# Performance work log

Hardware: AMD Instinct MI355X
Metric: run time of the kernel (lower is better)

## Reference

```python
import jax, jax.numpy as jnp
import numpy as np

NEG = -1000000000.0


def setup_inputs() -> dict:
    key = jax.random.key(0)
    k1, k2, k3, k4, k5 = jax.random.split(key, 5)
    B, T, D, Q = 8, 2048, 1024, 128
    x = jax.random.normal(k1, (B, T, D), dtype=jnp.float32)
    attn_mask = jax.random.randint(k2, (B, T), 0, 2).astype(jnp.bool_)
    s = 1.0 / np.sqrt(D)
    Wq = jax.random.normal(k3, (Q, D), dtype=jnp.float32) * s
    Wk = jax.random.normal(k4, (Q, D), dtype=jnp.float32) * s
    Wv = jax.random.normal(k5, (Q, D), dtype=jnp.float32) * s
    return {"x": x, "attn_mask": attn_mask, "Wq": Wq, "Wk": Wk, "Wv": Wv}


def reference(x, attn_mask, Wq, Wk, Wv):
    # x: (B,T,D); W*: (Q,D) torch Linear weights (y = x @ W.T)
    q = jnp.einsum('btd,qd->btq', x, Wq)
    k = jnp.einsum('btd,qd->btq', x, Wk)
    v = jnp.einsum('btd,qd->btq', x, Wv)
    logits = jnp.einsum('btq,bsq->bts', q, k)  # (B,T,T), no 1/sqrt(d) scaling (matches source)
    m = attn_mask[:, None, :]  # (B,1,T) broadcasts over query dim, == repeat(1,T,1)
    logits = jnp.where(m, logits, NEG)
    A = jax.nn.softmax(logits, axis=-1)
    A = jnp.where(m, A, 0.0)
    return jnp.einsum('bts,bsq->btq', A, v)
```

## Files before the change

### kernel.cpp

```cpp
#include <hip/hip_runtime.h>
#include <hip/hip_bf16.h>
#include <hip/hip_fp16.h>

typedef _Float16 half8 __attribute__((ext_vector_type(8)));
typedef _Float16 half4v __attribute__((ext_vector_type(4)));
typedef float float4v __attribute__((ext_vector_type(4)));

#define MFMA_F16(a, b, c) __builtin_amdgcn_mfma_f32_16x16x32_f16((a), (b), (c), 0, 0, 0)

#define GLDS16(gp, lp) \
    __builtin_amdgcn_global_load_lds((const __attribute__((address_space(1))) unsigned int*)(gp), \
                                     (__attribute__((address_space(3))) unsigned int*)(lp), 16, 0, 0)

#define BATCH 8
#define SEQ   2048
#define DIM   1024
#define QD    128
#define BT    (BATCH * SEQ)
#define NSPLIT 4
#define KSPAN (SEQ / NSPLIT)

__device__ __forceinline__ float dpp_max16(float x) {
    int v;
    v = __builtin_amdgcn_update_dpp(0, __float_as_int(x), 0xB1, 0xF, 0xF, false);
    x = fmaxf(x, __int_as_float(v));
    v = __builtin_amdgcn_update_dpp(0, __float_as_int(x), 0x4E, 0xF, 0xF, false);
    x = fmaxf(x, __int_as_float(v));
    v = __builtin_amdgcn_update_dpp(0, __float_as_int(x), 0x141, 0xF, 0xF, false);
    x = fmaxf(x, __int_as_float(v));
    v = __builtin_amdgcn_update_dpp(0, __float_as_int(x), 0x140, 0xF, 0xF, false);
    x = fmaxf(x, __int_as_float(v));
    return x;
}

__global__ __launch_bounds__(256) void cvt_w_kernel(const float* __restrict__ Wq,
                                                    const float* __restrict__ Wk,
                                                    const float* __restrict__ Wv,
                                                    _Float16* __restrict__ Wh) {
    const float* src = (blockIdx.y == 0) ? Wq : ((blockIdx.y == 1) ? Wk : Wv);
    int i = blockIdx.x * 256 + threadIdx.x;
    float4 f = ((const float4*)src)[i];
    half4v h = {(_Float16)f.x, (_Float16)f.y, (_Float16)f.z, (_Float16)f.w};
    ((half4v*)(Wh + (size_t)blockIdx.y * QD * DIM))[i] = h;
}

__global__ __launch_bounds__(512, 1) void proj_kernel(
    const float* __restrict__ x,
    const _Float16* __restrict__ Wh,
    _Float16* __restrict__ q_out,
    _Float16* __restrict__ k_out,
    _Float16* __restrict__ vt_out)
{
    __shared__ _Float16 As[2][64 * 64];
    __shared__ _Float16 Bs[2][3 * 128 * 64];

    const int tid  = threadIdx.x;
    const int lane = tid & 63;
    const int wave = tid >> 6;
    const int quad = lane >> 4;
    const int l15  = lane & 15;
    const int wr   = wave >> 2;
    const int wcg  = wave & 3;

    const int row0 = blockIdx.x * 64;

    const int ar  = tid >> 3;
    const int ac8 = tid & 7;
    const float* xp = x + (size_t)(row0 + ar) * DIM + ac8 * 8;
    const int aslot = ar * 64 + ((ac8 ^ (ar & 7)) * 8);

    float4v acc[3][2][2];
#pragma unroll
    for (int m = 0; m < 3; m++)
#pragma unroll
        for (int rf = 0; rf < 2; rf++)
#pragma unroll
            for (int nf = 0; nf < 2; nf++)
                acc[m][rf][nf] = (float4v){0.f, 0.f, 0.f, 0.f};

    {
        float4 a0 = *(const float4*)(xp + 0);
        float4 a1 = *(const float4*)(xp + 4);
#pragma unroll
        for (int c = 0; c < 6; c++) {
            int ci = c * 512 + tid;
            int m  = ci >> 10;
            int ri = (ci >> 3) & 127;
            int gs = ci & 7;
            int g  = gs ^ (ri & 7);
            GLDS16(Wh + (size_t)m * QD * DIM + (size_t)ri * DIM + g * 8, &Bs[0][ci * 8]);
        }
        half8 h;
        h[0] = (_Float16)a0.x; h[1] = (_Float16)a0.y; h[2] = (_Float16)a0.z; h[3] = (_Float16)a0.w;
        h[4] = (_Float16)a1.x; h[5] = (_Float16)a1.y; h[6] = (_Float16)a1.z; h[7] = (_Float16)a1.w;
        *(half8*)&As[0][aslot] = h;
    }
    __syncthreads();

    for (int t = 0; t < 16; t++) {
        const int cur = t & 1;
        const int nxt = cur ^ 1;

        float4 b0, b1;
        if (t < 15) {
            const float* xq = xp + (t + 1) * 64;
            b0 = *(const float4*)(xq + 0);
            b1 = *(const float4*)(xq + 4);
            const int kkn = (t + 1) * 64;
#pragma unroll
            for (int c = 0; c < 6; c++) {
                int ci = c * 512 + tid;
                int m  = ci >> 10;
                int ri = (ci >> 3) & 127;
                int gs = ci & 7;
                int g  = gs ^ (ri & 7);
                GLDS16(Wh + (size_t)m * QD * DIM + (size_t)ri * DIM + kkn + g * 8,
                       &Bs[nxt][ci * 8]);
            }
        }

        half8 af[2][2];
#pragma unroll
        for (int rf = 0; rf < 2; rf++)
#pragma unroll
            for (int kc = 0; kc < 2; kc++) {
                int r = wr * 32 + rf * 16 + l15;
                int g = (kc * 4 + quad) ^ (r & 7);
                af[rf][kc] = *(const half8*)&As[cur][r * 64 + g * 8];
            }
#pragma unroll
        for (int m = 0; m < 3; m++) {
            half8 bf[2][2];
#pragma unroll
            for (int nf = 0; nf < 2; nf++)
#pragma unroll
                for (int kc = 0; kc < 2; kc++) {
                    int r = wcg * 32 + nf * 16 + l15;
                    int g = (kc * 4 + quad) ^ (r & 7);
                    bf[nf][kc] = *(const half8*)&Bs[cur][m * 8192 + r * 64 + g * 8];
                }
#pragma unroll
            for (int kc = 0; kc < 2; kc++)
#pragma unroll
                for (int rf = 0; rf < 2; rf++)
#pragma unroll
                    for (int nf = 0; nf < 2; nf++)
                        acc[m][rf][nf] = MFMA_F16(af[rf][kc], bf[nf][kc], acc[m][rf][nf]);
        }

        if (t < 15) {
            half8 h;
            h[0] = (_Float16)b0.x; h[1] = (_Float16)b0.y; h[2] = (_Float16)b0.z; h[3] = (_Float16)b0.w;
            h[4] = (_Float16)b1.x; h[5] = (_Float16)b1.y; h[6] = (_Float16)b1.z; h[7] = (_Float16)b1.w;
            *(half8*)&As[nxt][aslot] = h;
        }
        __syncthreads();
    }

#pragma unroll
    for (int m = 0; m < 3; m++) {
        if (m == 2) {
#pragma unroll
            for (int rf = 0; rf < 2; rf++) {
                int grow0 = row0 + wr * 32 + rf * 16 + quad * 4;
                int b  = grow0 >> 11;
                int t0 = grow0 & 2047;
#pragma unroll
                for (int nf = 0; nf < 2; nf++) {
                    int col = wcg * 32 + nf * 16 + l15;
                    half4v h;
#pragma unroll
                    for (int r = 0; r < 4; r++) h[r] = (_Float16)acc[m][rf][nf][r];
                    *(half4v*)&vt_out[((size_t)(b * QD + col)) * SEQ + t0] = h;
                }
            }
        } else {
            _Float16* out = (m == 0) ? q_out : k_out;
#pragma unroll
            for (int rf = 0; rf < 2; rf++) {
                int grow0 = row0 + wr * 32 + rf * 16 + quad * 4;
#pragma unroll
                for (int nf = 0; nf < 2; nf++) {
                    int col = wcg * 32 + nf * 16 + l15;
#pragma unroll
                    for (int r = 0; r < 4; r++)
                        out[(size_t)(grow0 + r) * QD + col] = (_Float16)acc[m][rf][nf][r];
                }
            }
        }
    }
}

__global__ __launch_bounds__(256, 2) void attn_kernel(
    const _Float16* __restrict__ q,
    const _Float16* __restrict__ k,
    const _Float16* __restrict__ vt,
    const int* __restrict__ mask,
    _Float16* __restrict__ Op,
    float2* __restrict__ ml)
{
    __shared__ _Float16 Ks[64 * 128];
    __shared__ _Float16 Vs[128 * 64];
    __shared__ _Float16 Ps[4 * 32 * 64];
    __shared__ float Msf[64];

    const int tid  = threadIdx.x;
    const int lane = tid & 63;
    const int wave = tid >> 6;
    const int quad = lane >> 4;
    const int l15  = lane & 15;

    const int b  = blockIdx.y;
    const int z  = blockIdx.z;
    const int rowbase = blockIdx.x * 128 + wave * 32;

    half8 qf[2][4];
#pragma unroll
    for (int rf = 0; rf < 2; rf++) {
        const _Float16* qrow = q + ((size_t)(b * SEQ + rowbase + rf * 16 + l15)) * QD + quad * 8;
#pragma unroll
        for (int kc = 0; kc < 4; kc++)
            qf[rf][kc] = *(const half8*)(qrow + kc * 32);
    }

    const half8 onesv = {(_Float16)1, (_Float16)1, (_Float16)1, (_Float16)1,
                         (_Float16)1, (_Float16)1, (_Float16)1, (_Float16)1};

    float4v oacc[2][8];
#pragma unroll
    for (int rf = 0; rf < 2; rf++)
#pragma unroll
        for (int n = 0; n < 8; n++)
            oacc[rf][n] = (float4v){0.f, 0.f, 0.f, 0.f};
    float4v lacc[2] = {(float4v){0.f, 0.f, 0.f, 0.f}, (float4v){0.f, 0.f, 0.f, 0.f}};
    float mrow[2][4];
#pragma unroll
    for (int rf = 0; rf < 2; rf++)
#pragma unroll
        for (int r = 0; r < 4; r++) mrow[rf][r] = -1e30f;

    _Float16* Pw = &Ps[wave * 32 * 64];

    for (int sb = z * KSPAN; sb < z * KSPAN + KSPAN; sb += 64) {
        __syncthreads();
#pragma unroll
        for (int c = 0; c < 4; c++) {
            int ci = wave * 256 + c * 64 + lane;
            int r  = ci >> 4;
            int gs = ci & 15;
            int g  = (gs & 8) | ((gs ^ r) & 7);
            GLDS16(k + ((size_t)(b * SEQ + sb + r)) * QD + g * 8, &Ks[(wave * 256 + c * 64) * 8]);
        }
#pragma unroll
        for (int c = 0; c < 4; c++) {
            int ci = wave * 256 + c * 64 + lane;
            int r  = ci >> 3;
            int g  = ((ci & 7) ^ r) & 7;
            GLDS16(vt + ((size_t)(b * QD + r)) * SEQ + sb + g * 8, &Vs[(wave * 256 + c * 64) * 8]);
        }
        if (tid < 64) Msf[tid] = mask[b * SEQ + sb + tid] ? 0.f : -1e30f;
        __syncthreads();

        float4v sacc[2][4];
#pragma unroll
        for (int rf = 0; rf < 2; rf++)
#pragma unroll
            for (int j = 0; j < 4; j++)
                sacc[rf][j] = (float4v){0.f, 0.f, 0.f, 0.f};
#pragma unroll
        for (int kc = 0; kc < 4; kc++) {
            half8 kf[4];
#pragma unroll
            for (int j = 0; j < 4; j++) {
                int r  = j * 16 + l15;
                int g  = kc * 4 + quad;
                int gs = (g & 8) | ((g ^ r) & 7);
                kf[j] = *(const half8*)&Ks[r * 128 + gs * 8];
            }
#pragma unroll
            for (int rf = 0; rf < 2; rf++)
#pragma unroll
                for (int j = 0; j < 4; j++)
                    sacc[rf][j] = MFMA_F16(qf[rf][kc], kf[j], sacc[rf][j]);
        }

        float alpha[2][4];
#pragma unroll
        for (int rf = 0; rf < 2; rf++) {
            float rmax[4] = {-1e30f, -1e30f, -1e30f, -1e30f};
#pragma unroll
            for (int j = 0; j < 4; j++) {
                float bias = Msf[j * 16 + l15];
#pragma unroll
                for (int r = 0; r < 4; r++) {
                    float s = sacc[rf][j][r] + bias;
                    sacc[rf][j][r] = s;
                    rmax[r] = fmaxf(rmax[r], s);
                }
            }
#pragma unroll
            for (int r = 0; r < 4; r++) {
                float rm = dpp_max16(rmax[r]);
                float mnew = fmaxf(mrow[rf][r], rm);
                alpha[rf][r] = __expf(mrow[rf][r] - mnew);
                mrow[rf][r] = mnew;
            }
        }

#pragma unroll
        for (int rf = 0; rf < 2; rf++)
#pragma unroll
            for (int j = 0; j < 4; j++) {
                int col = j * 16 + l15;
                int gc  = col >> 3;
#pragma unroll
                for (int r = 0; r < 4; r++) {
                    int m  = rf * 16 + quad * 4 + r;
                    int gs = (gc ^ m) & 7;
                    float p = __expf(sacc[rf][j][r] - mrow[rf][r]);
                    Pw[m * 64 + gs * 8 + (col & 7)] = (_Float16)p;
                }
            }

#pragma unroll
        for (int rf = 0; rf < 2; rf++) {
#pragma unroll
            for (int n = 0; n < 8; n++)
#pragma unroll
                for (int r = 0; r < 4; r++)
                    oacc[rf][n][r] *= alpha[rf][r];
#pragma unroll
            for (int r = 0; r < 4; r++) lacc[rf][r] *= alpha[rf][r];
        }

#pragma unroll
        for (int kc = 0; kc < 2; kc++) {
            half8 pf[2];
#pragma unroll
            for (int rf = 0; rf < 2; rf++) {
                int m  = rf * 16 + l15;
                int gs = ((kc * 4 + quad) ^ m) & 7;
                pf[rf] = *(const half8*)&Pw[m * 64 + gs * 8];
            }
#pragma unroll
            for (int n = 0; n < 8; n++) {
                int r  = n * 16 + l15;
                int gs = ((kc * 4 + quad) ^ r) & 7;
                half8 vf = *(const half8*)&Vs[r * 64 + gs * 8];
#pragma unroll
                for (int rf = 0; rf < 2; rf++)
                    oacc[rf][n] = MFMA_F16(pf[rf], vf, oacc[rf][n]);
            }
#pragma unroll
            for (int rf = 0; rf < 2; rf++)
                lacc[rf] = MFMA_F16(pf[rf], onesv, lacc[rf]);
        }
    }

    _Float16* Oz = Op + (size_t)z * BT * QD;
#pragma unroll
    for (int rf = 0; rf < 2; rf++) {
#pragma unroll
        for (int n = 0; n < 8; n++) {
            int col = n * 16 + l15;
#pragma unroll
            for (int r = 0; r < 4; r++) {
                int row = rowbase + rf * 16 + quad * 4 + r;
                Oz[((size_t)(b * SEQ + row)) * QD + col] = (_Float16)oacc[rf][n][r];
            }
        }
        if (l15 == 0) {
#pragma unroll
            for (int r = 0; r < 4; r++) {
                int row = rowbase + rf * 16 + quad * 4 + r;
                ml[(size_t)z * BT + b * SEQ + row] = make_float2(mrow[rf][r], lacc[rf][r]);
            }
        }
    }
}

__global__ __launch_bounds__(256) void merge_kernel(
    const _Float16* __restrict__ Op,
    const float2* __restrict__ ml,
    float* __restrict__ out)
{
    int gid = blockIdx.x * 256 + threadIdx.x;
    int row = gid >> 4;
    int c8  = (gid & 15) * 8;

    float2 a[NSPLIT];
    float m = -3.0e38f;
#pragma unroll
    for (int s = 0; s < NSPLIT; s++) { a[s] = ml[(size_t)s * BT + row]; m = fmaxf(m, a[s].x); }
    float sc[NSPLIT];
    float denom = 0.f;
#pragma unroll
    for (int s = 0; s < NSPLIT; s++) { sc[s] = __expf(a[s].x - m); denom += sc[s] * a[s].y; }
    float inv = (denom > 0.f) ? (1.0f / denom) : 0.f;

    float acc[8] = {0, 0, 0, 0, 0, 0, 0, 0};
#pragma unroll
    for (int s = 0; s < NSPLIT; s++) {
        half8 o = *(const half8*)&Op[(size_t)s * BT * QD + (size_t)row * QD + c8];
#pragma unroll
        for (int e = 0; e < 8; e++) acc[e] += (float)o[e] * sc[s];
    }
    float4 lo = make_float4(acc[0] * inv, acc[1] * inv, acc[2] * inv, acc[3] * inv);
    float4 hi = make_float4(acc[4] * inv, acc[5] * inv, acc[6] * inv, acc[7] * inv);
    *(float4*)&out[(size_t)row * QD + c8] = lo;
    *(float4*)&out[(size_t)row * QD + c8 + 4] = hi;
}

extern "C" void kernel_launch(void* const* d_in, const int* in_sizes, int n_in,
                              void* d_out, int out_size, void* d_ws, size_t ws_size,
                              hipStream_t stream) {
    const float* x    = (const float*)d_in[0];
    const int*   mask = (const int*)d_in[1];
    const float* Wq   = (const float*)d_in[2];
    const float* Wk   = (const float*)d_in[3];
    const float* Wv   = (const float*)d_in[4];
    float* out = (float*)d_out;

    char* p = (char*)d_ws;
    _Float16* Wh  = (_Float16*)p; p += (size_t)3 * QD * DIM * 2;
    _Float16* qb  = (_Float16*)p; p += (size_t)BT * QD * 2;
    _Float16* kb  = (_Float16*)p; p += (size_t)BT * QD * 2;
    _Float16* vtb = (_Float16*)p; p += (size_t)BT * QD * 2;
    _Float16* Op  = (_Float16*)p; p += (size_t)NSPLIT * BT * QD * 2;
    float2*   ml  = (float2*)p;

    cvt_w_kernel<<<dim3(QD * DIM / 4 / 256, 3), 256, 0, stream>>>(Wq, Wk, Wv, Wh);
    proj_kernel<<<dim3(BT / 64), 512, 0, stream>>>(x, Wh, qb, kb, vtb);
    attn_kernel<<<dim3(SEQ / 128, BATCH, NSPLIT), 256, 0, stream>>>(qb, kb, vtb, mask, Op, ml);
    merge_kernel<<<dim3(BT * 16 / 256), 256, 0, stream>>>(Op, ml, out);
}
```

Baseline: 156.4 us.

## Double-buffer K and mask in attention and use fine-grained waitcnt barriers

```diff
diff --git a/kernel.cpp b/kernel.cpp
--- a/kernel.cpp
+++ b/kernel.cpp
@@ -11,6 +11,11 @@
 #define GLDS16(gp, lp) \
     __builtin_amdgcn_global_load_lds((const __attribute__((address_space(1))) unsigned int*)(gp), \
                                      (__attribute__((address_space(3))) unsigned int*)(lp), 16, 0, 0)
+
+#define WAITCNT_VM(N) asm volatile("s_waitcnt vmcnt(" #N ")" ::: "memory")
+#define WAITCNT_LGKM0() asm volatile("s_waitcnt lgkmcnt(0)" ::: "memory")
+#define SCHED_FENCE() __builtin_amdgcn_sched_barrier(0)
+#define BARRIER() __builtin_amdgcn_s_barrier()
 
 #define BATCH 8
 #define SEQ   2048
@@ -95,8 +100,10 @@
         h[4] = (_Float16)a1.x; h[5] = (_Float16)a1.y; h[6] = (_Float16)a1.z; h[7] = (_Float16)a1.w;
         *(half8*)&As[0][aslot] = h;
     }
-    __syncthreads();
-
+    WAITCNT_LGKM0();
+    BARRIER();
+
+#pragma unroll
     for (int t = 0; t < 16; t++) {
         const int cur = t & 1;
         const int nxt = cur ^ 1;
@@ -119,6 +126,9 @@
             }
         }
 
+        if (t < 15) { WAITCNT_VM(8); } else { WAITCNT_VM(0); }
+        SCHED_FENCE();
+
         half8 af[2][2];
 #pragma unroll
         for (int rf = 0; rf < 2; rf++)
@@ -153,8 +163,9 @@
             h[0] = (_Float16)b0.x; h[1] = (_Float16)b0.y; h[2] = (_Float16)b0.z; h[3] = (_Float16)b0.w;
             h[4] = (_Float16)b1.x; h[5] = (_Float16)b1.y; h[6] = (_Float16)b1.z; h[7] = (_Float16)b1.w;
             *(half8*)&As[nxt][aslot] = h;
-        }
-        __syncthreads();
+            WAITCNT_LGKM0();
+            BARRIER();
+        }
     }
 
 #pragma unroll
@@ -199,10 +210,10 @@
     _Float16* __restrict__ Op,
     float2* __restrict__ ml)
 {
-    __shared__ _Float16 Ks[64 * 128];
+    __shared__ _Float16 Ks[2][64 * 128];
     __shared__ _Float16 Vs[128 * 64];
     __shared__ _Float16 Ps[4 * 32 * 64];
-    __shared__ float Msf[64];
+    __shared__ float Msf[2][64];
 
     const int tid  = threadIdx.x;
     const int lane = tid & 63;
@@ -213,6 +224,7 @@
     const int b  = blockIdx.y;
     const int z  = blockIdx.z;
     const int rowbase = blockIdx.x * 128 + wave * 32;
+    const int sb0 = z * KSPAN;
 
     half8 qf[2][4];
 #pragma unroll
@@ -221,6 +233,13 @@
 #pragma unroll
         for (int kc = 0; kc < 4; kc++)
             qf[rf][kc] = *(const half8*)(qrow + kc * 32);
+    }
+
+    int mreg[8];
+    if (wave == 0) {
+#pragma unroll
+        for (int i = 0; i < 8; i++)
+            mreg[i] = mask[b * SEQ + sb0 + i * 64 + lane];
     }
 
     const half8 onesv = {(_Float16)1, (_Float16)1, (_Float16)1, (_Float16)1,
@@ -241,16 +260,24 @@
 
     _Float16* Pw = &Ps[wave * 32 * 64];
 
-    for (int sb = z * KSPAN; sb < z * KSPAN + KSPAN; sb += 64) {
-        __syncthreads();
-#pragma unroll
-        for (int c = 0; c < 4; c++) {
-            int ci = wave * 256 + c * 64 + lane;
-            int r  = ci >> 4;
-            int gs = ci & 15;
-            int g  = (gs & 8) | ((gs ^ r) & 7);
-            GLDS16(k + ((size_t)(b * SEQ + sb + r)) * QD + g * 8, &Ks[(wave * 256 + c * 64) * 8]);
-        }
+#pragma unroll
+    for (int c = 0; c < 4; c++) {
+        int ci = wave * 256 + c * 64 + lane;
+        int r  = ci >> 4;
+        int gs = ci & 15;
+        int g  = (gs & 8) | ((gs ^ r) & 7);
+        GLDS16(k + ((size_t)(b * SEQ + sb0 + r)) * QD + g * 8, &Ks[0][(wave * 256 + c * 64) * 8]);
+    }
+    if (wave == 0) Msf[0][lane] = mreg[0] ? 0.f : -1e30f;
+    WAITCNT_LGKM0();
+    BARRIER();
+
+#pragma unroll
+    for (int t = 0; t < 8; t++) {
+        const int cur = t & 1;
+        const int nxt = cur ^ 1;
+        const int sb  = sb0 + t * 64;
+
 #pragma unroll
         for (int c = 0; c < 4; c++) {
             int ci = wave * 256 + c * 64 + lane;
@@ -258,8 +285,21 @@
             int g  = ((ci & 7) ^ r) & 7;
             GLDS16(vt + ((size_t)(b * QD + r)) * SEQ + sb + g * 8, &Vs[(wave * 256 + c * 64) * 8]);
         }
-        if (tid < 64) Msf[tid] = mask[b * SEQ + sb + tid] ? 0.f : -1e30f;
-        __syncthreads();
+        if (t < 7) {
+            if (wave == 0) Msf[nxt][lane] = mreg[t + 1] ? 0.f : -1e30f;
+#pragma unroll
+            for (int c = 0; c < 4; c++) {
+                int ci = wave * 256 + c * 64 + lane;
+                int r  = ci >> 4;
+                int gs = ci & 15;
+                int g  = (gs & 8) | ((gs ^ r) & 7);
+                GLDS16(k + ((size_t)(b * SEQ + sb + 64 + r)) * QD + g * 8,
+                       &Ks[nxt][(wave * 256 + c * 64) * 8]);
+            }
+        }
+
+        if (t < 7) { WAITCNT_VM(8); } else { WAITCNT_VM(4); }
+        SCHED_FENCE();
 
         float4v sacc[2][4];
 #pragma unroll
@@ -275,7 +315,7 @@
                 int r  = j * 16 + l15;
                 int g  = kc * 4 + quad;
                 int gs = (g & 8) | ((g ^ r) & 7);
-                kf[j] = *(const half8*)&Ks[r * 128 + gs * 8];
+                kf[j] = *(const half8*)&Ks[cur][r * 128 + gs * 8];
             }
 #pragma unroll
             for (int rf = 0; rf < 2; rf++)
@@ -290,7 +330,7 @@
             float rmax[4] = {-1e30f, -1e30f, -1e30f, -1e30f};
 #pragma unroll
             for (int j = 0; j < 4; j++) {
-                float bias = Msf[j * 16 + l15];
+                float bias = Msf[cur][j * 16 + l15];
 #pragma unroll
                 for (int r = 0; r < 4; r++) {
                     float s = sacc[rf][j][r] + bias;
@@ -333,6 +373,9 @@
             for (int r = 0; r < 4; r++) lacc[rf][r] *= alpha[rf][r];
         }
 
+        if (t < 7) { WAITCNT_VM(4); } else { WAITCNT_VM(0); }
+        SCHED_FENCE();
+
 #pragma unroll
         for (int kc = 0; kc < 2; kc++) {
             half8 pf[2];
@@ -354,6 +397,11 @@
 #pragma unroll
             for (int rf = 0; rf < 2; rf++)
                 lacc[rf] = MFMA_F16(pf[rf], onesv, lacc[rf]);
+        }
+
+        if (t < 7) {
+            WAITCNT_LGKM0();
+            BARRIER();
         }
     }
 
```

New measurement: 156.1 us. About the same (-0.2%).

## Load x directly into MFMA fragment registers and relax projection loop barriers

Applied to the files above, without the earlier changes.

```diff
diff --git a/kernel.cpp b/kernel.cpp
--- a/kernel.cpp
+++ b/kernel.cpp
@@ -11,6 +11,10 @@
 #define GLDS16(gp, lp) \
     __builtin_amdgcn_global_load_lds((const __attribute__((address_space(1))) unsigned int*)(gp), \
                                      (__attribute__((address_space(3))) unsigned int*)(lp), 16, 0, 0)
+
+#define WAITCNT_VM(N) asm volatile("s_waitcnt vmcnt(" #N ")" ::: "memory")
+#define SCHED_FENCE() __builtin_amdgcn_sched_barrier(0)
+#define BARRIER() __builtin_amdgcn_s_barrier()
 
 #define BATCH 8
 #define SEQ   2048
@@ -51,7 +55,6 @@
     _Float16* __restrict__ k_out,
     _Float16* __restrict__ vt_out)
 {
-    __shared__ _Float16 As[2][64 * 64];
     __shared__ _Float16 Bs[2][3 * 128 * 64];
 
     const int tid  = threadIdx.x;
@@ -64,10 +67,7 @@
 
     const int row0 = blockIdx.x * 64;
 
-    const int ar  = tid >> 3;
-    const int ac8 = tid & 7;
-    const float* xp = x + (size_t)(row0 + ar) * DIM + ac8 * 8;
-    const int aslot = ar * 64 + ((ac8 ^ (ar & 7)) * 8);
+    const float* xr0 = x + (size_t)(row0 + wr * 32 + l15) * DIM + quad * 8;
 
     float4v acc[3][2][2];
 #pragma unroll
@@ -78,42 +78,41 @@
             for (int nf = 0; nf < 2; nf++)
                 acc[m][rf][nf] = (float4v){0.f, 0.f, 0.f, 0.f};
 
-    {
-        float4 a0 = *(const float4*)(xp + 0);
-        float4 a1 = *(const float4*)(xp + 4);
-#pragma unroll
-        for (int c = 0; c < 6; c++) {
-            int ci = c * 512 + tid;
-            int m  = ci >> 10;
-            int ri = (ci >> 3) & 127;
-            int gs = ci & 7;
-            int g  = gs ^ (ri & 7);
-            GLDS16(Wh + (size_t)m * QD * DIM + (size_t)ri * DIM + g * 8, &Bs[0][ci * 8]);
-        }
-        half8 h;
-        h[0] = (_Float16)a0.x; h[1] = (_Float16)a0.y; h[2] = (_Float16)a0.z; h[3] = (_Float16)a0.w;
-        h[4] = (_Float16)a1.x; h[5] = (_Float16)a1.y; h[6] = (_Float16)a1.z; h[7] = (_Float16)a1.w;
-        *(half8*)&As[0][aslot] = h;
-    }
-    __syncthreads();
-
+    float4 ax[2][2][2];
+
+#pragma unroll
+    for (int c = 0; c < 6; c++) {
+        int ci = c * 512 + tid;
+        int m  = ci >> 10;
+        int ri = (ci >> 3) & 127;
+        int g  = (ci & 7) ^ (ri & 7);
+        GLDS16(Wh + (size_t)m * QD * DIM + (size_t)ri * DIM + g * 8, &Bs[0][ci * 8]);
+    }
+#pragma unroll
+    for (int rf = 0; rf < 2; rf++)
+#pragma unroll
+        for (int kc = 0; kc < 2; kc++) {
+            const float* p = xr0 + rf * 16 * DIM + kc * 32;
+            ax[rf][kc][0] = *(const float4*)(p + 0);
+            ax[rf][kc][1] = *(const float4*)(p + 4);
+        }
+    WAITCNT_VM(8);
+    SCHED_FENCE();
+    BARRIER();
+
+#pragma unroll
     for (int t = 0; t < 16; t++) {
         const int cur = t & 1;
         const int nxt = cur ^ 1;
 
-        float4 b0, b1;
         if (t < 15) {
-            const float* xq = xp + (t + 1) * 64;
-            b0 = *(const float4*)(xq + 0);
-            b1 = *(const float4*)(xq + 4);
             const int kkn = (t + 1) * 64;
 #pragma unroll
             for (int c = 0; c < 6; c++) {
                 int ci = c * 512 + tid;
                 int m  = ci >> 10;
                 int ri = (ci >> 3) & 127;
-                int gs = ci & 7;
-                int g  = gs ^ (ri & 7);
+                int g  = (ci & 7) ^ (ri & 7);
                 GLDS16(Wh + (size_t)m * QD * DIM + (size_t)ri * DIM + kkn + g * 8,
                        &Bs[nxt][ci * 8]);
             }
@@ -124,10 +123,26 @@
         for (int rf = 0; rf < 2; rf++)
 #pragma unroll
             for (int kc = 0; kc < 2; kc++) {
-                int r = wr * 32 + rf * 16 + l15;
-                int g = (kc * 4 + quad) ^ (r & 7);
-                af[rf][kc] = *(const half8*)&As[cur][r * 64 + g * 8];
-            }
+                half8 h;
+                h[0] = (_Float16)ax[rf][kc][0].x; h[1] = (_Float16)ax[rf][kc][0].y;
+                h[2] = (_Float16)ax[rf][kc][0].z; h[3] = (_Float16)ax[rf][kc][0].w;
+                h[4] = (_Float16)ax[rf][kc][1].x; h[5] = (_Float16)ax[rf][kc][1].y;
+                h[6] = (_Float16)ax[rf][kc][1].z; h[7] = (_Float16)ax[rf][kc][1].w;
+                af[rf][kc] = h;
+            }
+
+        if (t < 15) {
+            const float* xk = xr0 + (t + 1) * 64;
+#pragma unroll
+            for (int rf = 0; rf < 2; rf++)
+#pragma unroll
+                for (int kc = 0; kc < 2; kc++) {
+                    const float* p = xk + rf * 16 * DIM + kc * 32;
+                    ax[rf][kc][0] = *(const float4*)(p + 0);
+                    ax[rf][kc][1] = *(const float4*)(p + 4);
+                }
+        }
+
 #pragma unroll
         for (int m = 0; m < 3; m++) {
             half8 bf[2][2];
@@ -149,12 +164,11 @@
         }
 
         if (t < 15) {
-            half8 h;
-            h[0] = (_Float16)b0.x; h[1] = (_Float16)b0.y; h[2] = (_Float16)b0.z; h[3] = (_Float16)b0.w;
-            h[4] = (_Float16)b1.x; h[5] = (_Float16)b1.y; h[6] = (_Float16)b1.z; h[7] = (_Float16)b1.w;
-            *(half8*)&As[nxt][aslot] = h;
-        }
-        __syncthreads();
+            asm volatile("s_waitcnt lgkmcnt(0)" ::: "memory");
+            WAITCNT_VM(8);
+            SCHED_FENCE();
+            BARRIER();
+        }
     }
 
 #pragma unroll
```

New measurement: 179.3 us. 14.6% more time.

## Split projection output columns across two blocks to raise occupancy

Applied to the files above, without the earlier changes.

```diff
diff --git a/kernel.cpp b/kernel.cpp
--- a/kernel.cpp
+++ b/kernel.cpp
@@ -44,7 +44,7 @@
     ((half4v*)(Wh + (size_t)blockIdx.y * QD * DIM))[i] = h;
 }
 
-__global__ __launch_bounds__(512, 1) void proj_kernel(
+__global__ __launch_bounds__(512, 4) void proj_kernel(
     const float* __restrict__ x,
     const _Float16* __restrict__ Wh,
     _Float16* __restrict__ q_out,
@@ -52,7 +52,7 @@
     _Float16* __restrict__ vt_out)
 {
     __shared__ _Float16 As[2][64 * 64];
-    __shared__ _Float16 Bs[2][3 * 128 * 64];
+    __shared__ _Float16 Bs[2][192 * 64];
 
     const int tid  = threadIdx.x;
     const int lane = tid & 63;
@@ -63,32 +63,31 @@
     const int wcg  = wave & 3;
 
     const int row0 = blockIdx.x * 64;
+    const int ch   = blockIdx.y;
 
     const int ar  = tid >> 3;
     const int ac8 = tid & 7;
     const float* xp = x + (size_t)(row0 + ar) * DIM + ac8 * 8;
     const int aslot = ar * 64 + ((ac8 ^ (ar & 7)) * 8);
 
-    float4v acc[3][2][2];
-#pragma unroll
-    for (int m = 0; m < 3; m++)
-#pragma unroll
-        for (int rf = 0; rf < 2; rf++)
-#pragma unroll
-            for (int nf = 0; nf < 2; nf++)
-                acc[m][rf][nf] = (float4v){0.f, 0.f, 0.f, 0.f};
+    float4v acc[2][3];
+#pragma unroll
+    for (int rf = 0; rf < 2; rf++)
+#pragma unroll
+        for (int nf = 0; nf < 3; nf++)
+            acc[rf][nf] = (float4v){0.f, 0.f, 0.f, 0.f};
 
     {
         float4 a0 = *(const float4*)(xp + 0);
         float4 a1 = *(const float4*)(xp + 4);
 #pragma unroll
-        for (int c = 0; c < 6; c++) {
+        for (int c = 0; c < 3; c++) {
             int ci = c * 512 + tid;
-            int m  = ci >> 10;
-            int ri = (ci >> 3) & 127;
-            int gs = ci & 7;
-            int g  = gs ^ (ri & 7);
-            GLDS16(Wh + (size_t)m * QD * DIM + (size_t)ri * DIM + g * 8, &Bs[0][ci * 8]);
+            int ri = ci >> 3;
+            int m  = ri >> 6;
+            int wrow = ch * 64 + (ri & 63);
+            int g  = (ci & 7) ^ (ri & 7);
+            GLDS16(Wh + (size_t)m * QD * DIM + (size_t)wrow * DIM + g * 8, &Bs[0][ci * 8]);
         }
         half8 h;
         h[0] = (_Float16)a0.x; h[1] = (_Float16)a0.y; h[2] = (_Float16)a0.z; h[3] = (_Float16)a0.w;
@@ -108,13 +107,13 @@
             b1 = *(const float4*)(xq + 4);
             const int kkn = (t + 1) * 64;
 #pragma unroll
-            for (int c = 0; c < 6; c++) {
+            for (int c = 0; c < 3; c++) {
                 int ci = c * 512 + tid;
-                int m  = ci >> 10;
-                int ri = (ci >> 3) & 127;
-                int gs = ci & 7;
-                int g  = gs ^ (ri & 7);
-                GLDS16(Wh + (size_t)m * QD * DIM + (size_t)ri * DIM + kkn + g * 8,
+                int ri = ci >> 3;
+                int m  = ri >> 6;
+                int wrow = ch * 64 + (ri & 63);
+                int g  = (ci & 7) ^ (ri & 7);
+                GLDS16(Wh + (size_t)m * QD * DIM + (size_t)wrow * DIM + kkn + g * 8,
                        &Bs[nxt][ci * 8]);
             }
         }
@@ -128,64 +127,52 @@
                 int g = (kc * 4 + quad) ^ (r & 7);
                 af[rf][kc] = *(const half8*)&As[cur][r * 64 + g * 8];
             }
-#pragma unroll
-        for (int m = 0; m < 3; m++) {
-            half8 bf[2][2];
-#pragma unroll
-            for (int nf = 0; nf < 2; nf++)
-#pragma unroll
-                for (int kc = 0; kc < 2; kc++) {
-                    int r = wcg * 32 + nf * 16 + l15;
-                    int g = (kc * 4 + quad) ^ (r & 7);
-                    bf[nf][kc] = *(const half8*)&Bs[cur][m * 8192 + r * 64 + g * 8];
-                }
-#pragma unroll
-            for (int kc = 0; kc < 2; kc++)
-#pragma unroll
-                for (int rf = 0; rf < 2; rf++)
-#pragma unroll
-                    for (int nf = 0; nf < 2; nf++)
-                        acc[m][rf][nf] = MFMA_F16(af[rf][kc], bf[nf][kc], acc[m][rf][nf]);
-        }
+        half8 bf[3][2];
+#pragma unroll
+        for (int nf = 0; nf < 3; nf++)
+#pragma unroll
+            for (int kc = 0; kc < 2; kc++) {
+                int r = wcg * 48 + nf * 16 + l15;
+                int g = (kc * 4 + quad) ^ (r & 7);
+                bf[nf][kc] = *(const half8*)&Bs[cur][r * 64 + g * 8];
+            }
+#pragma unroll
+        for (int kc = 0; kc < 2; kc++)
+#pragma unroll
+            for (int rf = 0; rf < 2; rf++)
+#pragma unroll
+                for (int nf = 0; nf < 3; nf++)
+                    acc[rf][nf] = MFMA_F16(af[rf][kc], bf[nf][kc], acc[rf][nf]);
 
         if (t < 15) {
             half8 h;
             h[0] = (_Float16)b0.x; h[1] = (_Float16)b0.y; h[2] = (_Float16)b0.z; h[3] = (_Float16)b0.w;
             h[4] = (_Float16)b1.x; h[5] = (_Float16)b1.y; h[6] = (_Float16)b1.z; h[7] = (_Float16)b1.w;
             *(half8*)&As[nxt][aslot] = h;
-        }
-        __syncthreads();
-    }
-
-#pragma unroll
-    for (int m = 0; m < 3; m++) {
-        if (m == 2) {
-#pragma unroll
-            for (int rf = 0; rf < 2; rf++) {
-                int grow0 = row0 + wr * 32 + rf * 16 + quad * 4;
-                int b  = grow0 >> 11;
-                int t0 = grow0 & 2047;
-#pragma unroll
-                for (int nf = 0; nf < 2; nf++) {
-                    int col = wcg * 32 + nf * 16 + l15;
-                    half4v h;
-#pragma unroll
-                    for (int r = 0; r < 4; r++) h[r] = (_Float16)acc[m][rf][nf][r];
-                    *(half4v*)&vt_out[((size_t)(b * QD + col)) * SEQ + t0] = h;
-                }
-            }
-        } else {
-            _Float16* out = (m == 0) ? q_out : k_out;
-#pragma unroll
-            for (int rf = 0; rf < 2; rf++) {
-                int grow0 = row0 + wr * 32 + rf * 16 + quad * 4;
-#pragma unroll
-                for (int nf = 0; nf < 2; nf++) {
-                    int col = wcg * 32 + nf * 16 + l15;
-#pragma unroll
-                    for (int r = 0; r < 4; r++)
-                        out[(size_t)(grow0 + r) * QD + col] = (_Float16)acc[m][rf][nf][r];
-                }
+            __syncthreads();
+        }
+    }
+
+#pragma unroll
+    for (int rf = 0; rf < 2; rf++) {
+        int grow0 = row0 + wr * 32 + rf * 16 + quad * 4;
+        int b  = grow0 >> 11;
+        int t0 = grow0 & 2047;
+#pragma unroll
+        for (int nf = 0; nf < 3; nf++) {
+            int col192 = wcg * 48 + nf * 16 + l15;
+            int m   = col192 >> 6;
+            int col = ch * 64 + (col192 & 63);
+            if (m == 2) {
+                half4v h;
+#pragma unroll
+                for (int r = 0; r < 4; r++) h[r] = (_Float16)acc[rf][nf][r];
+                *(half4v*)&vt_out[((size_t)(b * QD + col)) * SEQ + t0] = h;
+            } else {
+                _Float16* out = (m == 0) ? q_out : k_out;
+#pragma unroll
+                for (int r = 0; r < 4; r++)
+                    out[(size_t)(grow0 + r) * QD + col] = (_Float16)acc[rf][nf][r];
             }
         }
     }
@@ -430,7 +417,7 @@
     float2*   ml  = (float2*)p;
 
     cvt_w_kernel<<<dim3(QD * DIM / 4 / 256, 3), 256, 0, stream>>>(Wq, Wk, Wv, Wh);
-    proj_kernel<<<dim3(BT / 64), 512, 0, stream>>>(x, Wh, qb, kb, vtb);
+    proj_kernel<<<dim3(BT / 64, 2), 512, 0, stream>>>(x, Wh, qb, kb, vtb);
     attn_kernel<<<dim3(SEQ / 128, BATCH, NSPLIT), 256, 0, stream>>>(qb, kb, vtb, mask, Op, ml);
     merge_kernel<<<dim3(BT * 16 / 256), 256, 0, stream>>>(Op, ml, out);
 }
```

Measured after the change: 155.2 us (median of 2 runs). Within noise of the previous version (-0.8%).
